# Kernel tuning notes

Hardware: AMD Instinct MI355X
Metric: run time of the kernel (lower is better)

Reference implementation:

```python
import jax, jax.numpy as jnp
from jax import lax
import numpy as np

B, N, CF = 16, 4096, 64
NPOINT, NSAMPLE = 1024, 32
MLP = (64, 64, 128)
IN_CH = CF + 3
EPS = 1e-5


def _fps(xyz, npoint):
    # Farthest point sampling; deterministic start at index 0 (original uses a random start).
    Bn = xyz.shape[0]
    d0 = jnp.full(xyz.shape[:2], 1e10, xyz.dtype)
    f0 = jnp.zeros((Bn,), jnp.int32)
    def step(carry, _):
        dist, far = carry
        c = jnp.take_along_axis(xyz, far[:, None, None], axis=1)  # (B,1,3)
        d = jnp.sum((xyz - c) ** 2, axis=-1)                      # (B,N)
        dist = jnp.minimum(dist, d)
        return (dist, jnp.argmax(dist, axis=1).astype(jnp.int32)), far
    _, idxs = lax.scan(step, (d0, f0), None, length=npoint)
    return jnp.transpose(idxs)  # (B, npoint)


def _gather(pts, idx):
    # pts (B,N,C), idx (B,...) int -> (B,...,C)
    return jax.vmap(lambda p, i: p[i])(pts, idx)


def _bn_relu(x, g, b, axes):
    # training-mode batch norm (batch statistics), channel axis = 1
    m = jnp.mean(x, axes, keepdims=True)
    v = jnp.var(x, axes, keepdims=True)
    sh = (1, -1) + (1,) * (x.ndim - 2)
    return jax.nn.relu((x - m) * lax.rsqrt(v + EPS) * g.reshape(sh) + b.reshape(sh))


def _forward(xyz, points, density, params):
    fps_idx = _fps(xyz, NPOINT)
    new_xyz = _gather(xyz, fps_idx)  # (B,S,3)
    # source query_ball_point sorts distances and keeps the nsample nearest -> kNN
    d = (jnp.sum(new_xyz ** 2, -1)[:, :, None] + jnp.sum(xyz ** 2, -1)[:, None, :]
         - 2.0 * jnp.einsum('bsc,bnc->bsn', new_xyz, xyz))  # (B,S,N)
    _, idx = lax.top_k(-d, NSAMPLE)  # (B,S,ns) nearest neighbors
    gxyz = _gather(xyz, idx) - new_xyz[:, :, None, :]           # (B,S,ns,3)
    gpts = _gather(jnp.transpose(points, (0, 2, 1)), idx)       # (B,S,ns,CF)
    x = jnp.transpose(jnp.concatenate([gxyz, gpts], -1), (0, 3, 1, 2))  # (B,IN_CH,S,ns)
    (w0, b0, g0, be0, w1, b1, g1, be1, w2, b2, g2, be2, wd, bd, gd, bed) = params
    for w, b, g, be in ((w0, b0, g0, be0), (w1, b1, g1, be1), (w2, b2, g2, be2)):
        x = _bn_relu(jnp.einsum('oc,bcsk->bosk', w, x) + b[None, :, None, None], g, be, (0, 2, 3))
    # density weighting at sampled centers
    dcen = jnp.transpose(_gather(jnp.transpose(density, (0, 2, 1)), fps_idx), (0, 2, 1))  # (B,1,S)
    dw = _bn_relu(jnp.einsum('oc,bcs->bos', wd, dcen) + bd[None, :, None], gd, bed, (0, 2))  # (B,Cout,S)
    x = x * dw[..., None]
    return new_xyz, jnp.max(x, axis=-1)  # (B,S,3), (B,Cout,S)


def setup_inputs() -> dict:
    key = jax.random.key(0)
    ks = jax.random.split(key, 3)
    inp = {
        'xyz': jax.random.normal(ks[0], (B, N, 3), jnp.float32),
        'points': jax.random.normal(ks[1], (B, CF, N), jnp.float32),
        'density': jax.random.uniform(ks[2], (B, 1, N), jnp.float32),
    }
    chans = (IN_CH,) + MLP
    for i in range(3):
        cin, cout = chans[i], chans[i + 1]
        inp[f'w{i}'] = jax.random.normal(jax.random.fold_in(key, 10 + i), (cout, cin), jnp.float32) / np.sqrt(cin).astype(np.float32)
        inp[f'b{i}'] = jnp.zeros((cout,), jnp.float32)
        inp[f'g{i}'] = jnp.ones((cout,), jnp.float32)
        inp[f'be{i}'] = jnp.zeros((cout,), jnp.float32)
    inp['wd'] = jax.random.normal(jax.random.fold_in(key, 20), (MLP[-1], 1), jnp.float32)
    inp['bd'] = jnp.zeros((MLP[-1],), jnp.float32)
    inp['gd'] = jnp.ones((MLP[-1],), jnp.float32)
    inp['bed'] = jnp.zeros((MLP[-1],), jnp.float32)
    return inp


def reference(xyz, points, density, w0, b0, g0, be0, w1, b1, g1, be1, w2, b2, g2, be2, wd, bd, gd, bed):
    return _forward(xyz, points, density,
                    (w0, b0, g0, be0, w1, b1, g1, be1, w2, b2, g2, be2, wd, bd, gd, bed))
```

## Files before the change

### kernel.cpp

```cpp
#include <hip/hip_runtime.h>
#include <hip/hip_bf16.h>
#include <stdint.h>

#define NB 16
#define NN 4096
#define NCF 64
#define NS 1024
#define NK 32
#define NPTS (NB*NS*NK)
#define CIN 67
#define EPSV 1e-5f

static __device__ __forceinline__ float fmul(float a, float b){ return __fmul_rn(a,b); }
static __device__ __forceinline__ float fadd(float a, float b){ return __fadd_rn(a,b); }
static __device__ __forceinline__ float fsub(float a, float b){ return __fsub_rn(a,b); }

typedef float f2 __attribute__((ext_vector_type(2)));
#define PK_ADD(d,a,b) asm("v_pk_add_f32 %0, %1, %2" : "=v"(d) : "v"(a), "v"(b))
#define PK_MUL(d,a,b) asm("v_pk_mul_f32 %0, %1, %2" : "=v"(d) : "v"(a), "v"(b))
static __device__ __forceinline__ f2 pk_add(f2 a, f2 b){ f2 d; PK_ADD(d,a,b); return d; }

typedef short bf16x8 __attribute__((ext_vector_type(8)));
typedef float f32x4 __attribute__((ext_vector_type(4)));

static __device__ __forceinline__ unsigned short f2b(float f){
  unsigned u = __float_as_uint(f);
  return (unsigned short)((u + 0x7FFFu + ((u>>16)&1u)) >> 16);
}
static __device__ __forceinline__ unsigned pack2(float a, float b){
  return (unsigned)f2b(a) | ((unsigned)f2b(b)<<16);
}
static __device__ __forceinline__ unsigned long long umax64(unsigned long long a,
                                                            unsigned long long b){
  return a > b ? a : b;
}

template<int CTRL>
static __device__ __forceinline__ float dppmax_f32(float x){
  float o = __uint_as_float((unsigned)__builtin_amdgcn_update_dpp(
      0, (int)__float_as_uint(x), CTRL, 0xf, 0xf, true));
  return fmaxf(x, o);
}
static __device__ __forceinline__ float wave_max63_f32(float x){
  x = dppmax_f32<0x111>(x); x = dppmax_f32<0x112>(x);
  x = dppmax_f32<0x114>(x); x = dppmax_f32<0x118>(x);
  x = dppmax_f32<0x142>(x); x = dppmax_f32<0x143>(x);
  return x;
}
template<int CTRL>
static __device__ __forceinline__ float dppmax_keep(float x){
  float o = __uint_as_float((unsigned)__builtin_amdgcn_update_dpp(
      (int)__float_as_uint(x), (int)__float_as_uint(x), CTRL, 0xf, 0xf, false));
  return fmaxf(x, o);
}
static __device__ __forceinline__ float row16_max_f32(float x){
  x = dppmax_keep<0x111>(x); x = dppmax_keep<0x112>(x);
  x = dppmax_keep<0x114>(x); x = dppmax_keep<0x118>(x);
  return x;
}
template<int CTRL>
static __device__ __forceinline__ f2 dppadd_f2(f2 x){
  f2 o;
  o.x = __uint_as_float((unsigned)__builtin_amdgcn_update_dpp(
      0, (int)__float_as_uint(x.x), CTRL, 0xf, 0xf, true));
  o.y = __uint_as_float((unsigned)__builtin_amdgcn_update_dpp(
      0, (int)__float_as_uint(x.y), CTRL, 0xf, 0xf, true));
  return pk_add(x, o);
}
static __device__ __forceinline__ f2 row16_sum_f2(f2 x){
  x = dppadd_f2<0x111>(x); x = dppadd_f2<0x112>(x);
  x = dppadd_f2<0x114>(x); x = dppadd_f2<0x118>(x);
  return x;
}
static __device__ __forceinline__ unsigned long long readlane_u64(unsigned long long v, int l){
  unsigned lo = (unsigned)__builtin_amdgcn_readlane((int)(unsigned)v, l);
  unsigned hi = (unsigned)__builtin_amdgcn_readlane((int)(unsigned)(v>>32), l);
  return ((unsigned long long)hi<<32) | lo;
}
static __device__ __forceinline__ unsigned long long wave_shr1_u64(unsigned long long x){
  unsigned lo = (unsigned)__builtin_amdgcn_update_dpp(
      0, (int)(unsigned)x, 0x138, 0xf, 0xf, true);
  unsigned hi = (unsigned)__builtin_amdgcn_update_dpp(
      0, (int)(unsigned)(x>>32), 0x138, 0xf, 0xf, true);
  return ((unsigned long long)hi<<32) | lo;
}

__global__ __launch_bounds__(256) void prep_kernel(const float* __restrict__ pts,
    const float* __restrict__ xyz, unsigned short* __restrict__ ptsT,
    float* __restrict__ sqx){
  int blk = blockIdx.x;
  int b = blk >> 4;
  int n = ((blk & 15) << 8) + threadIdx.x;
  const float* src = pts + (size_t)b*NCF*NN + n;
  float v[NCF];
  #pragma unroll
  for (int c=0;c<NCF;c++) v[c] = src[(size_t)c*NN];
  uint4* dst = (uint4*)(ptsT + ((size_t)b*NN + n)*NCF);
  #pragma unroll
  for (int j=0;j<8;j++)
    dst[j] = make_uint4(pack2(v[8*j],v[8*j+1]), pack2(v[8*j+2],v[8*j+3]),
                        pack2(v[8*j+4],v[8*j+5]), pack2(v[8*j+6],v[8*j+7]));
  const float* xp = xyz + ((size_t)b*NN + n)*3;
  float x=xp[0], y=xp[1], z=xp[2];
  sqx[(size_t)b*NN+n] = fadd(fadd(fmul(x,x),fmul(y,y)),fmul(z,z));
}

#define FT 512
__global__ __launch_bounds__(FT) void fps_kernel(const float* __restrict__ xyz,
    int* __restrict__ fidx, float* __restrict__ newxyz){
  int b = blockIdx.x;
  __shared__ float4 s4[NN];
  __shared__ unsigned long long candK[2][8];
  const int tid = threadIdx.x;
  const int lane = tid & 63;
  const int wv = tid >> 6;
  for (int i = tid; i < NN; i += FT){
    const float* p = xyz + ((size_t)b*NN + i)*3;
    s4[i] = make_float4(p[0], p[1], p[2], 0.f);
  }
  __syncthreads();
  f2 px[4], py[4], pz[4], d2[4];
  #pragma unroll
  for (int m=0;m<4;m++){
    float4 a = s4[tid*8 + 2*m];
    float4 c = s4[tid*8 + 2*m + 1];
    px[m] = (f2){a.x, c.x};
    py[m] = (f2){a.y, c.y};
    pz[m] = (f2){a.z, c.z};
    d2[m] = (f2){1e10f, 1e10f};
  }
  int far = 0;
  float4 cc = s4[0];
  for (int s=0;s<NS;s++){
    if (tid==0){
      fidx[b*NS+s] = far;
      float* o = newxyz + ((size_t)b*NS+s)*3;
      o[0]=cc.x; o[1]=cc.y; o[2]=cc.z;
    }
    f2 ncx = (f2){-cc.x,-cc.x}, ncy = (f2){-cc.y,-cc.y}, ncz = (f2){-cc.z,-cc.z};
    float bv = -1.0f; int bj = 0;
    #pragma unroll
    for (int m=0;m<4;m++){
      f2 dx,dy,dz,xx,yy,zz,ss,dd;
      PK_ADD(dx, px[m], ncx);
      PK_ADD(dy, py[m], ncy);
      PK_ADD(dz, pz[m], ncz);
      PK_MUL(xx, dx, dx);
      PK_MUL(yy, dy, dy);
      PK_ADD(ss, xx, yy);
      PK_MUL(zz, dz, dz);
      PK_ADD(dd, ss, zz);
      float u0 = fminf(d2[m].x, dd.x);
      float u1 = fminf(d2[m].y, dd.y);
      d2[m].x = u0; d2[m].y = u1;
      if (u0 > bv){ bv = u0; bj = 2*m; }
      if (u1 > bv){ bv = u1; bj = 2*m+1; }
    }
    int nbest = (tid<<3) + bj;
    float mv = wave_max63_f32(bv);
    float mvu = __uint_as_float((unsigned)__builtin_amdgcn_readlane(
        (int)__float_as_uint(mv), 63));
    unsigned long long tiedm = __ballot(bv == mvu);
    int wl = __ffsll(tiedm) - 1;
    unsigned nwin = (unsigned)__builtin_amdgcn_readlane(nbest, wl);
    if (lane == 0)
      candK[s&1][wv] = ((unsigned long long)__float_as_uint(mvu) << 32)
                     | (unsigned long long)(unsigned)~nwin;
    __syncthreads();
    const ulonglong2* cp = (const ulonglong2*)candK[s&1];
    ulonglong2 c0=cp[0], c1=cp[1], c2=cp[2], c3=cp[3];
    unsigned long long kk = umax64(
        umax64(umax64(c0.x,c0.y), umax64(c1.x,c1.y)),
        umax64(umax64(c2.x,c2.y), umax64(c3.x,c3.y)));
    far = (int)(~(unsigned)kk) & (NN-1);
    cc = s4[far];
  }
}

__global__ __launch_bounds__(256) void dcen_kernel(const float* __restrict__ density,
    const int* __restrict__ fidx, float* __restrict__ dcen){
  int i = blockIdx.x*256 + threadIdx.x;
  int b = i >> 10;
  dcen[i] = density[(size_t)b*NN + fidx[i]];
}

__global__ __launch_bounds__(256) void dstats_kernel(const float* __restrict__ dcen,
    float* __restrict__ dstat){
  float s=0.f, q=0.f;
  for (int i=threadIdx.x; i<NB*NS; i+=256){ float v=dcen[i]; s+=v; q+=v*v; }
  __shared__ float ls[256], lq[256];
  ls[threadIdx.x]=s; lq[threadIdx.x]=q;
  __syncthreads();
  for (int off=128; off>0; off>>=1){
    if (threadIdx.x<off){ ls[threadIdx.x]+=ls[threadIdx.x+off]; lq[threadIdx.x]+=lq[threadIdx.x+off]; }
    __syncthreads();
  }
  if (threadIdx.x==0){
    float m = ls[0]/(float)(NB*NS);
    dstat[0]=m; dstat[1]=lq[0]/(float)(NB*NS) - m*m;
  }
}

__global__ __launch_bounds__(256) void knn_kernel(const float* __restrict__ xyz,
    const float* __restrict__ sqx, const float* __restrict__ newxyz,
    int* __restrict__ kidx){
  const int lane = threadIdx.x & 63;
  const int g = blockIdx.x*4 + (threadIdx.x >> 6);
  const int b = g >> 10;
  const float* cp = newxyz + (size_t)g*3;
  const float cx=cp[0], cy=cp[1], cz=cp[2];
  const float sqc = fadd(fadd(fmul(cx,cx),fmul(cy,cy)),fmul(cz,cz));
  const float* xb  = xyz + (size_t)b*NN*3;
  const float* sqb = sqx + (size_t)b*NN;
  unsigned long long kept  = ~0ULL;
  unsigned long long worst = ~0ULL;
  for (int n0=0; n0<NN; n0+=64){
    const int n = n0 + lane;
    const float* xp = xb + (size_t)n*3;
    float x=xp[0], y=xp[1], z=xp[2];
    float dot = fadd(fadd(fmul(cx,x),fmul(cy,y)),fmul(cz,z));
    float d = fsub(fadd(sqc, sqb[n]), fmul(2.0f,dot));
    unsigned u = __float_as_uint(d);
    u = (u & 0x80000000u) ? ~u : (u | 0x80000000u);
    unsigned long long ck = ((unsigned long long)u << 32) | (unsigned)n;
    unsigned long long mask = __ballot(ck < worst);
    while (mask){
      const int l = __ffsll(mask) - 1;
      mask &= mask - 1;
      const unsigned long long k = readlane_u64(ck, l);
      if (k < worst){
        bool m = kept > k;
        unsigned long long M = __ballot(m) << 1;
        unsigned long long sh = wave_shr1_u64(kept);
        bool msh = (M >> lane) & 1ULL;
        unsigned long long ins = msh ? sh : k;
        kept = m ? ins : kept;
        worst = readlane_u64(kept, 31);
      }
    }
  }
  if (lane < 32) kidx[(size_t)g*NK + lane] = (int)(kept & 0xFFFFFFFFULL);
}


__global__ __launch_bounds__(256) void conv1_kernel(const float* __restrict__ xyz,
    const unsigned short* __restrict__ ptsT, const float* __restrict__ newxyz,
    const int* __restrict__ kidx, const float* __restrict__ w0,
    const float* __restrict__ b0, unsigned short* __restrict__ z1,
    float* __restrict__ partial){
  __shared__ unsigned short sa[128][104];
  __shared__ unsigned short swb[64][104];
  const int tid = threadIdx.x;
  const int p0 = blockIdx.x * 128;
  for (int i = tid; i < 64*52; i += 256){
    int o = i / 52, pr = i - o*52, c0 = 2*pr;
    float v0 = (c0 < 64) ? w0[o*CIN + 3 + c0] : (c0 < 67 ? w0[o*CIN + (c0-64)] : 0.f);
    int c1 = c0 + 1;
    float v1 = (c1 < 64) ? w0[o*CIN + 3 + c1] : (c1 < 67 ? w0[o*CIN + (c1-64)] : 0.f);
    *(unsigned*)&swb[o][c0] = pack2(v0, v1);
  }
  #pragma unroll
  for (int j=0;j<4;j++){
    int idx = tid + j*256;
    int pt = idx >> 3, cg = idx & 7;
    int p = p0 + pt, g = p >> 5, b = g >> 10;
    int n = kidx[p];
    uint4 vv = *(const uint4*)(ptsT + ((size_t)b*NN + n)*NCF + cg*8);
    *(uint4*)&sa[pt][cg*8] = vv;
  }
  if (tid < 128){
    int p = p0 + tid, g = p >> 5, b = g >> 10;
    int n = kidx[p];
    const float* xp = xyz + ((size_t)b*NN + n)*3;
    const float* cp = newxyz + (size_t)g*3;
    float gx = xp[0]-cp[0], gy = xp[1]-cp[1], gz = xp[2]-cp[2];
    *(uint2*)&sa[tid][64] = make_uint2(pack2(gx,gy), pack2(gz,0.f));
    *(uint2*)&sa[tid][68] = make_uint2(0u,0u);
    uint4 zz = make_uint4(0u,0u,0u,0u);
    *(uint4*)&sa[tid][72] = zz; *(uint4*)&sa[tid][80] = zz;
    *(uint4*)&sa[tid][88] = zz; *(uint4*)&sa[tid][96] = zz;
  }
  __syncthreads();
  const int wv = tid >> 6, lane = tid & 63;
  const int r15 = lane & 15, q = lane >> 4;
  f32x4 acc[8];
  #pragma unroll
  for (int t=0;t<8;t++) acc[t] = (f32x4){0.f,0.f,0.f,0.f};
  #pragma unroll
  for (int ks=0; ks<3; ks++){
    bf16x8 af = *(const bf16x8*)&swb[wv*16 + r15][ks*32 + q*8];
    #pragma unroll
    for (int t=0;t<8;t++){
      bf16x8 bfr = *(const bf16x8*)&sa[t*16 + r15][ks*32 + q*8];
      acc[t] = __builtin_amdgcn_mfma_f32_16x16x32_bf16(af, bfr, acc[t], 0,0,0);
    }
  }
  float bias[4];
  #pragma unroll
  for (int r=0;r<4;r++) bias[r] = b0[wv*16 + q*4 + r];
  f2 st[4];
  #pragma unroll
  for (int r=0;r<4;r++) st[r] = (f2){0.f,0.f};
  #pragma unroll
  for (int t=0;t<8;t++){
    float z0=acc[t][0]+bias[0], z1v=acc[t][1]+bias[1];
    float z2v=acc[t][2]+bias[2], z3v=acc[t][3]+bias[3];
    st[0] = pk_add(st[0], (f2){z0, z0*z0});
    st[1] = pk_add(st[1], (f2){z1v, z1v*z1v});
    st[2] = pk_add(st[2], (f2){z2v, z2v*z2v});
    st[3] = pk_add(st[3], (f2){z3v, z3v*z3v});
    *(uint2*)(z1 + (size_t)(p0 + t*16 + r15)*64 + wv*16 + q*4)
        = make_uint2(pack2(z0,z1v), pack2(z2v,z3v));
  }
  #pragma unroll
  for (int r=0;r<4;r++){
    f2 s = row16_sum_f2(st[r]);
    if (r15 == 15){
      int ch = wv*16 + q*4 + r;
      partial[(size_t)blockIdx.x*128 + ch] = s.x;
      partial[(size_t)blockIdx.x*128 + 64 + ch] = s.y;
    }
  }
}

__global__ __launch_bounds__(256) void conv2_kernel(const unsigned short* __restrict__ z1,
    const float* __restrict__ w1, const float* __restrict__ b1,
    const float* __restrict__ scale1, const float* __restrict__ shift1,
    unsigned short* __restrict__ z2, float* __restrict__ partial){
  __shared__ unsigned short sa[128][72];
  __shared__ unsigned short swb[64][72];
  const int tid = threadIdx.x;
  const int p0 = blockIdx.x * 128;
  for (int i = tid; i < 64*32; i += 256){
    int o = i >> 5, c0 = (i & 31)*2;
    *(unsigned*)&swb[o][c0] = pack2(w1[o*64+c0], w1[o*64+c0+1]);
  }
  #pragma unroll
  for (int j=0;j<4;j++){
    int idx = tid + j*256;
    int pt = idx >> 3, cg = idx & 7;
    uint4 vv = *(const uint4*)(z1 + (size_t)(p0+pt)*64 + cg*8);
    unsigned a[4] = {vv.x, vv.y, vv.z, vv.w};
    unsigned r[4];
    #pragma unroll
    for (int t=0;t<4;t++){
      int c = cg*8 + t*2;
      float lo = __uint_as_float(a[t] << 16);
      float hi = __uint_as_float(a[t] & 0xFFFF0000u);
      float alo = fmaxf(lo*scale1[c]   + shift1[c],   0.f);
      float ahi = fmaxf(hi*scale1[c+1] + shift1[c+1], 0.f);
      r[t] = pack2(alo, ahi);
    }
    *(uint4*)&sa[pt][cg*8] = make_uint4(r[0],r[1],r[2],r[3]);
  }
  __syncthreads();
  const int wv = tid >> 6, lane = tid & 63;
  const int r15 = lane & 15, q = lane >> 4;
  f32x4 acc[8];
  #pragma unroll
  for (int t=0;t<8;t++) acc[t] = (f32x4){0.f,0.f,0.f,0.f};
  #pragma unroll
  for (int ks=0; ks<2; ks++){
    bf16x8 af = *(const bf16x8*)&swb[wv*16 + r15][ks*32 + q*8];
    #pragma unroll
    for (int t=0;t<8;t++){
      bf16x8 bfr = *(const bf16x8*)&sa[t*16 + r15][ks*32 + q*8];
      acc[t] = __builtin_amdgcn_mfma_f32_16x16x32_bf16(af, bfr, acc[t], 0,0,0);
    }
  }
  float bias[4];
  #pragma unroll
  for (int r=0;r<4;r++) bias[r] = b1[wv*16 + q*4 + r];
  f2 st[4];
  #pragma unroll
  for (int r=0;r<4;r++) st[r] = (f2){0.f,0.f};
  #pragma unroll
  for (int t=0;t<8;t++){
    float z0=acc[t][0]+bias[0], z1v=acc[t][1]+bias[1];
    float z2v=acc[t][2]+bias[2], z3v=acc[t][3]+bias[3];
    st[0] = pk_add(st[0], (f2){z0, z0*z0});
    st[1] = pk_add(st[1], (f2){z1v, z1v*z1v});
    st[2] = pk_add(st[2], (f2){z2v, z2v*z2v});
    st[3] = pk_add(st[3], (f2){z3v, z3v*z3v});
    *(uint2*)(z2 + (size_t)(p0 + t*16 + r15)*64 + wv*16 + q*4)
        = make_uint2(pack2(z0,z1v), pack2(z2v,z3v));
  }
  #pragma unroll
  for (int r=0;r<4;r++){
    f2 s = row16_sum_f2(st[r]);
    if (r15 == 15){
      int ch = wv*16 + q*4 + r;
      partial[(size_t)blockIdx.x*128 + ch] = s.x;
      partial[(size_t)blockIdx.x*128 + 64 + ch] = s.y;
    }
  }
}

__global__ __launch_bounds__(256) void conv3_kernel(const unsigned short* __restrict__ z2,
    const float* __restrict__ w2, const float* __restrict__ b2,
    const float* __restrict__ scale2, const float* __restrict__ shift2,
    float* __restrict__ m3, float* __restrict__ partial){
  __shared__ unsigned short sa[128][72];
  __shared__ unsigned short swb[128][72];
  const int tid = threadIdx.x;
  const int p0 = blockIdx.x * 128;
  for (int i = tid; i < 128*32; i += 256){
    int o = i >> 5, c0 = (i & 31)*2;
    *(unsigned*)&swb[o][c0] = pack2(w2[o*64+c0], w2[o*64+c0+1]);
  }
  #pragma unroll
  for (int j=0;j<4;j++){
    int idx = tid + j*256;
    int pt = idx >> 3, cg = idx & 7;
    uint4 vv = *(const uint4*)(z2 + (size_t)(p0+pt)*64 + cg*8);
    unsigned a[4] = {vv.x, vv.y, vv.z, vv.w};
    unsigned r[4];
    #pragma unroll
    for (int t=0;t<4;t++){
      int c = cg*8 + t*2;
      float lo = __uint_as_float(a[t] << 16);
      float hi = __uint_as_float(a[t] & 0xFFFF0000u);
      float alo = fmaxf(lo*scale2[c]   + shift2[c],   0.f);
      float ahi = fmaxf(hi*scale2[c+1] + shift2[c+1], 0.f);
      r[t] = pack2(alo, ahi);
    }
    *(uint4*)&sa[pt][cg*8] = make_uint4(r[0],r[1],r[2],r[3]);
  }
  __syncthreads();
  const int wv = tid >> 6, lane = tid & 63;
  const int r15 = lane & 15, q = lane >> 4;
  f32x4 acc[2][8];
  #pragma unroll
  for (int mm=0;mm<2;mm++)
    #pragma unroll
    for (int t=0;t<8;t++) acc[mm][t] = (f32x4){0.f,0.f,0.f,0.f};
  #pragma unroll
  for (int ks=0; ks<2; ks++){
    bf16x8 af0 = *(const bf16x8*)&swb[(wv*2+0)*16 + r15][ks*32 + q*8];
    bf16x8 af1 = *(const bf16x8*)&swb[(wv*2+1)*16 + r15][ks*32 + q*8];
    #pragma unroll
    for (int t=0;t<8;t++){
      bf16x8 bfr = *(const bf16x8*)&sa[t*16 + r15][ks*32 + q*8];
      acc[0][t] = __builtin_amdgcn_mfma_f32_16x16x32_bf16(af0, bfr, acc[0][t], 0,0,0);
      acc[1][t] = __builtin_amdgcn_mfma_f32_16x16x32_bf16(af1, bfr, acc[1][t], 0,0,0);
    }
  }
  #pragma unroll
  for (int mm=0;mm<2;mm++){
    const int base = (wv*2+mm)*16;
    float bias[4];
    #pragma unroll
    for (int r=0;r<4;r++) bias[r] = b2[base + q*4 + r];
    float zv[8][4];
    f2 st[4];
    #pragma unroll
    for (int r=0;r<4;r++) st[r] = (f2){0.f,0.f};
    #pragma unroll
    for (int t=0;t<8;t++){
      #pragma unroll
      for (int r=0;r<4;r++){
        float z = acc[mm][t][r] + bias[r];
        zv[t][r] = z;
        st[r] = pk_add(st[r], (f2){z, z*z});
      }
    }
    #pragma unroll
    for (int r=0;r<4;r++){
      f2 s = row16_sum_f2(st[r]);
      if (r15 == 15){
        int ch = base + q*4 + r;
        partial[(size_t)blockIdx.x*256 + ch] = s.x;
        partial[(size_t)blockIdx.x*256 + 128 + ch] = s.y;
      }
    }
    #pragma unroll
    for (int c=0;c<4;c++){
      #pragma unroll
      for (int r=0;r<4;r++){
        float m = row16_max_f32(fmaxf(zv[2*c][r], zv[2*c+1][r]));
        if (r15 == 15)
          m3[(size_t)(blockIdx.x*4 + c)*128 + base + q*4 + r] = m;
      }
    }
  }
}

__global__ __launch_bounds__(256) void mkbn_kernel(const float* __restrict__ partial,
    int nrows, int stride, const float* __restrict__ g, const float* __restrict__ be,
    float* __restrict__ scale, float* __restrict__ shift, float inv_count){
  const int c = blockIdx.x;
  const int C = gridDim.x;
  float s=0.f, q=0.f;
  for (int r=threadIdx.x; r<nrows; r+=256){
    s += partial[(size_t)r*stride + c];
    q += partial[(size_t)r*stride + C + c];
  }
  __shared__ float ls[256], lq[256];
  ls[threadIdx.x]=s; lq[threadIdx.x]=q;
  __syncthreads();
  for (int off=128; off>0; off>>=1){
    if (threadIdx.x < off){ ls[threadIdx.x]+=ls[threadIdx.x+off]; lq[threadIdx.x]+=lq[threadIdx.x+off]; }
    __syncthreads();
  }
  if (threadIdx.x==0){
    float mean = ls[0]*inv_count;
    float var  = lq[0]*inv_count - mean*mean;
    float sc = g[c]*rsqrtf(var + EPSV);
    scale[c]=sc; shift[c]=be[c]-mean*sc;
  }
}

__global__ __launch_bounds__(256) void final_kernel(const float* __restrict__ m3,
    const float* __restrict__ dcen, const float* __restrict__ scale3,
    const float* __restrict__ shift3, const float* __restrict__ wd,
    const float* __restrict__ bd, const float* __restrict__ gd,
    const float* __restrict__ bed, const float* __restrict__ dstat,
    float* __restrict__ out){
  size_t i = (size_t)blockIdx.x*256 + threadIdx.x;
  int s  = (int)(i & 1023);
  int ch = (int)((i >> 10) & 127);
  int b  = (int)(i >> 17);
  float mean_d = dstat[0], var_d = dstat[1];
  float w = wd[ch];
  float meanp = w*mean_d + bd[ch];
  float varp  = w*w*var_d;
  float dsc = gd[ch]*rsqrtf(varp + EPSV);
  float dsh = bed[ch] - meanp*dsc;
  float pre = w*dcen[b*NS+s] + bd[ch];
  float dw  = fmaxf(dsc*pre + dsh, 0.0f);
  float z   = m3[((size_t)(b*NS+s))*128 + ch];
  float x   = fmaxf(scale3[ch]*z + shift3[ch], 0.0f);
  out[i] = x*dw;
}

extern "C" void kernel_launch(void* const* d_in, const int* in_sizes, int n_in,
                              void* d_out, int out_size, void* d_ws, size_t ws_size,
                              hipStream_t stream){
  const float* xyz     = (const float*)d_in[0];
  const float* points  = (const float*)d_in[1];
  const float* density = (const float*)d_in[2];
  const float* w0 = (const float*)d_in[3];
  const float* b0 = (const float*)d_in[4];
  const float* g0 = (const float*)d_in[5];
  const float* be0= (const float*)d_in[6];
  const float* w1 = (const float*)d_in[7];
  const float* b1 = (const float*)d_in[8];
  const float* g1 = (const float*)d_in[9];
  const float* be1= (const float*)d_in[10];
  const float* w2 = (const float*)d_in[11];
  const float* b2 = (const float*)d_in[12];
  const float* g2 = (const float*)d_in[13];
  const float* be2= (const float*)d_in[14];
  const float* wd = (const float*)d_in[15];
  const float* bd = (const float*)d_in[16];
  const float* gd = (const float*)d_in[17];
  const float* bed= (const float*)d_in[18];

  float* out = (float*)d_out;
  float* newxyz = out;
  float* out1   = out + (size_t)NB*NS*3;

  unsigned short* ptsT = (unsigned short*)d_ws;
  float* sqx  = (float*)(ptsT + (size_t)NB*NN*NCF);
  int*   fidx = (int*)(sqx + (size_t)NB*NN);
  float* dcen = (float*)(fidx + NB*NS);
  int*   kidx = (int*)(dcen + NB*NS);
  unsigned short* z1 = (unsigned short*)(kidx + NPTS);
  unsigned short* z2 = z1 + (size_t)NPTS*64;
  float* m3   = (float*)(z2 + (size_t)NPTS*64);
  float* p1   = m3 + (size_t)NB*NS*128;
  float* p2   = p1 + 4096*128;
  float* p3   = p2 + 4096*128;
  float* bnp  = p3 + 4096*256;
  float* dstat= bnp + 512;

  hipLaunchKernelGGL(prep_kernel,  dim3(256),  dim3(256), 0, stream, points, xyz, ptsT, sqx);
  hipLaunchKernelGGL(fps_kernel,   dim3(NB),   dim3(FT),  0, stream, xyz, fidx, newxyz);
  hipLaunchKernelGGL(dcen_kernel,  dim3(64),   dim3(256), 0, stream, density, fidx, dcen);
  hipLaunchKernelGGL(dstats_kernel,dim3(1),    dim3(256), 0, stream, dcen, dstat);
  hipLaunchKernelGGL(knn_kernel,   dim3(4096), dim3(256), 0, stream, xyz, sqx, newxyz, kidx);
  hipLaunchKernelGGL(conv1_kernel, dim3(4096), dim3(256), 0, stream, xyz, ptsT, newxyz, kidx, w0, b0, z1, p1);
  hipLaunchKernelGGL(mkbn_kernel,  dim3(64),   dim3(256), 0, stream, p1, 4096, 128, g0, be0, bnp+0,   bnp+64,  1.0f/(float)NPTS);
  hipLaunchKernelGGL(conv2_kernel, dim3(4096), dim3(256), 0, stream, z1, w1, b1, bnp+0, bnp+64, z2, p2);
  hipLaunchKernelGGL(mkbn_kernel,  dim3(64),   dim3(256), 0, stream, p2, 4096, 128, g1, be1, bnp+128, bnp+192, 1.0f/(float)NPTS);
  hipLaunchKernelGGL(conv3_kernel, dim3(4096), dim3(256), 0, stream, z2, w2, b2, bnp+128, bnp+192, m3, p3);
  hipLaunchKernelGGL(mkbn_kernel,  dim3(128),  dim3(256), 0, stream, p3, 4096, 256, g2, be2, bnp+256, bnp+384, 1.0f/(float)NPTS);
  hipLaunchKernelGGL(final_kernel, dim3(8192), dim3(256), 0, stream, m3, dcen, bnp+256, bnp+384, wd, bd, gd, bed, dstat, out1);
}
```

Measured before the change: 1.137 ms.

## Shrink FPS block, carry winner coords via readlane, prepack bf16 weights, transpose m3

The FPS kernel drops to 256 threads with 16 points each. The winning point's coordinates are now passed through the shared candidate records, which removes the dependent shared-memory load of s4[far] on the serial critical path. Conv weights are converted to bf16 once in a new wprep kernel, so each of the 4096 conv blocks no longer repacks them. The m3 buffer is stored channel-major so the final kernel reads it coalesced, at the cost of scattered writes in conv3.

```diff
diff --git a/kernel.cpp b/kernel.cpp
--- a/kernel.cpp
+++ b/kernel.cpp
@@ -30,9 +30,8 @@
 static __device__ __forceinline__ unsigned pack2(float a, float b){
   return (unsigned)f2b(a) | ((unsigned)f2b(b)<<16);
 }
-static __device__ __forceinline__ unsigned long long umax64(unsigned long long a,
-                                                            unsigned long long b){
-  return a > b ? a : b;
+static __device__ __forceinline__ float readlane_f32(float v, int l){
+  return __uint_as_float((unsigned)__builtin_amdgcn_readlane((int)__float_as_uint(v), l));
 }
 
 template<int CTRL>
@@ -105,12 +104,29 @@
   sqx[(size_t)b*NN+n] = fadd(fadd(fmul(x,x),fmul(y,y)),fmul(z,z));
 }
 
-#define FT 512
+__global__ __launch_bounds__(256) void wprep_kernel(const float* __restrict__ w0,
+    const float* __restrict__ w1, const float* __restrict__ w2,
+    unsigned short* __restrict__ w0p, unsigned short* __restrict__ w1p,
+    unsigned short* __restrict__ w2p){
+  const int tid = threadIdx.x;
+  for (int i = tid; i < 64*128; i += 256){
+    int o = i >> 7, c = i & 127;
+    float v = 0.f;
+    if (c < 64) v = w0[o*CIN + 3 + c];
+    else if (c < 67) v = w0[o*CIN + (c-64)];
+    w0p[i] = f2b(v);
+  }
+  for (int i = tid; i < 64*64; i += 256)  w1p[i] = f2b(w1[i]);
+  for (int i = tid; i < 128*64; i += 256) w2p[i] = f2b(w2[i]);
+}
+
+#define FT 256
 __global__ __launch_bounds__(FT) void fps_kernel(const float* __restrict__ xyz,
     int* __restrict__ fidx, float* __restrict__ newxyz){
   int b = blockIdx.x;
   __shared__ float4 s4[NN];
-  __shared__ unsigned long long candK[2][8];
+  __shared__ ulonglong2 candA[2][4];
+  __shared__ float4 candZ[2];
   const int tid = threadIdx.x;
   const int lane = tid & 63;
   const int wv = tid >> 6;
@@ -119,28 +135,28 @@
     s4[i] = make_float4(p[0], p[1], p[2], 0.f);
   }
   __syncthreads();
-  f2 px[4], py[4], pz[4], d2[4];
-  #pragma unroll
-  for (int m=0;m<4;m++){
-    float4 a = s4[tid*8 + 2*m];
-    float4 c = s4[tid*8 + 2*m + 1];
+  f2 px[8], py[8], pz[8], d2[8];
+  #pragma unroll
+  for (int m=0;m<8;m++){
+    float4 a = s4[tid*16 + 2*m];
+    float4 c = s4[tid*16 + 2*m + 1];
     px[m] = (f2){a.x, c.x};
     py[m] = (f2){a.y, c.y};
     pz[m] = (f2){a.z, c.z};
     d2[m] = (f2){1e10f, 1e10f};
   }
   int far = 0;
-  float4 cc = s4[0];
+  float ccx = s4[0].x, ccy = s4[0].y, ccz = s4[0].z;
   for (int s=0;s<NS;s++){
     if (tid==0){
       fidx[b*NS+s] = far;
       float* o = newxyz + ((size_t)b*NS+s)*3;
-      o[0]=cc.x; o[1]=cc.y; o[2]=cc.z;
-    }
-    f2 ncx = (f2){-cc.x,-cc.x}, ncy = (f2){-cc.y,-cc.y}, ncz = (f2){-cc.z,-cc.z};
+      o[0]=ccx; o[1]=ccy; o[2]=ccz;
+    }
+    f2 ncx = (f2){-ccx,-ccx}, ncy = (f2){-ccy,-ccy}, ncz = (f2){-ccz,-ccz};
     float bv = -1.0f; int bj = 0;
     #pragma unroll
-    for (int m=0;m<4;m++){
+    for (int m=0;m<8;m++){
       f2 dx,dy,dz,xx,yy,zz,ss,dd;
       PK_ADD(dx, px[m], ncx);
       PK_ADD(dy, py[m], ncy);
@@ -156,24 +172,56 @@
       if (u0 > bv){ bv = u0; bj = 2*m; }
       if (u1 > bv){ bv = u1; bj = 2*m+1; }
     }
-    int nbest = (tid<<3) + bj;
+    int nbest = (tid<<4) + bj;
     float mv = wave_max63_f32(bv);
-    float mvu = __uint_as_float((unsigned)__builtin_amdgcn_readlane(
-        (int)__float_as_uint(mv), 63));
+    float mvu = readlane_f32(mv, 63);
     unsigned long long tiedm = __ballot(bv == mvu);
     int wl = __ffsll(tiedm) - 1;
     unsigned nwin = (unsigned)__builtin_amdgcn_readlane(nbest, wl);
-    if (lane == 0)
-      candK[s&1][wv] = ((unsigned long long)__float_as_uint(mvu) << 32)
-                     | (unsigned long long)(unsigned)~nwin;
+    int bjw = (int)(nwin & 15);
+    int mW = bjw >> 1;
+    f2 pxw, pyw, pzw;
+    switch(mW){
+      case 0: pxw=px[0]; pyw=py[0]; pzw=pz[0]; break;
+      case 1: pxw=px[1]; pyw=py[1]; pzw=pz[1]; break;
+      case 2: pxw=px[2]; pyw=py[2]; pzw=pz[2]; break;
+      case 3: pxw=px[3]; pyw=py[3]; pzw=pz[3]; break;
+      case 4: pxw=px[4]; pyw=py[4]; pzw=pz[4]; break;
+      case 5: pxw=px[5]; pyw=py[5]; pzw=pz[5]; break;
+      case 6: pxw=px[6]; pyw=py[6]; pzw=pz[6]; break;
+      default: pxw=px[7]; pyw=py[7]; pzw=pz[7]; break;
+    }
+    bool hi = (bjw & 1) != 0;
+    float cxw = readlane_f32(hi ? pxw.y : pxw.x, wl);
+    float cyw = readlane_f32(hi ? pyw.y : pyw.x, wl);
+    float czw = readlane_f32(hi ? pzw.y : pzw.x, wl);
+    if (lane == 0){
+      unsigned long long key = ((unsigned long long)__float_as_uint(mvu) << 32)
+                             | (unsigned long long)(unsigned)~nwin;
+      unsigned long long cxy = ((unsigned long long)__float_as_uint(cyw) << 32)
+                             | (unsigned long long)__float_as_uint(cxw);
+      candA[s&1][wv] = (ulonglong2){key, cxy};
+      ((float*)&candZ[s&1])[wv] = czw;
+    }
     __syncthreads();
-    const ulonglong2* cp = (const ulonglong2*)candK[s&1];
-    ulonglong2 c0=cp[0], c1=cp[1], c2=cp[2], c3=cp[3];
-    unsigned long long kk = umax64(
-        umax64(umax64(c0.x,c0.y), umax64(c1.x,c1.y)),
-        umax64(umax64(c2.x,c2.y), umax64(c3.x,c3.y)));
+    ulonglong2 A0 = candA[s&1][0], A1 = candA[s&1][1];
+    ulonglong2 A2 = candA[s&1][2], A3 = candA[s&1][3];
+    float4 Z = candZ[s&1];
+    bool a01 = A1.x > A0.x;
+    unsigned long long k01 = a01 ? A1.x : A0.x;
+    unsigned long long xy01 = a01 ? A1.y : A0.y;
+    float z01 = a01 ? Z.y : Z.x;
+    bool a23 = A3.x > A2.x;
+    unsigned long long k23 = a23 ? A3.x : A2.x;
+    unsigned long long xy23 = a23 ? A3.y : A2.y;
+    float z23 = a23 ? Z.w : Z.z;
+    bool af = k23 > k01;
+    unsigned long long kk = af ? k23 : k01;
+    unsigned long long xyf = af ? xy23 : xy01;
+    ccz = af ? z23 : z01;
+    ccx = __uint_as_float((unsigned)xyf);
+    ccy = __uint_as_float((unsigned)(xyf >> 32));
     far = (int)(~(unsigned)kk) & (NN-1);
-    cc = s4[far];
   }
 }
 
@@ -245,19 +293,17 @@
 
 __global__ __launch_bounds__(256) void conv1_kernel(const float* __restrict__ xyz,
     const unsigned short* __restrict__ ptsT, const float* __restrict__ newxyz,
-    const int* __restrict__ kidx, const float* __restrict__ w0,
+    const int* __restrict__ kidx, const unsigned short* __restrict__ w0p,
     const float* __restrict__ b0, unsigned short* __restrict__ z1,
     float* __restrict__ partial){
   __shared__ unsigned short sa[128][104];
   __shared__ unsigned short swb[64][104];
   const int tid = threadIdx.x;
   const int p0 = blockIdx.x * 128;
-  for (int i = tid; i < 64*52; i += 256){
-    int o = i / 52, pr = i - o*52, c0 = 2*pr;
-    float v0 = (c0 < 64) ? w0[o*CIN + 3 + c0] : (c0 < 67 ? w0[o*CIN + (c0-64)] : 0.f);
-    int c1 = c0 + 1;
-    float v1 = (c1 < 64) ? w0[o*CIN + 3 + c1] : (c1 < 67 ? w0[o*CIN + (c1-64)] : 0.f);
-    *(unsigned*)&swb[o][c0] = pack2(v0, v1);
+  for (int i = tid; i < 64*64; i += 256){
+    int o = i >> 6, c0 = (i & 63)*2;
+    if (c0 < 104)
+      *(unsigned*)&swb[o][c0] = *(const unsigned*)&w0p[o*128 + c0];
   }
   #pragma unroll
   for (int j=0;j<4;j++){
@@ -324,7 +370,7 @@
 }
 
 __global__ __launch_bounds__(256) void conv2_kernel(const unsigned short* __restrict__ z1,
-    const float* __restrict__ w1, const float* __restrict__ b1,
+    const unsigned short* __restrict__ w1p, const float* __restrict__ b1,
     const float* __restrict__ scale1, const float* __restrict__ shift1,
     unsigned short* __restrict__ z2, float* __restrict__ partial){
   __shared__ unsigned short sa[128][72];
@@ -333,7 +379,7 @@
   const int p0 = blockIdx.x * 128;
   for (int i = tid; i < 64*32; i += 256){
     int o = i >> 5, c0 = (i & 31)*2;
-    *(unsigned*)&swb[o][c0] = pack2(w1[o*64+c0], w1[o*64+c0+1]);
+    *(unsigned*)&swb[o][c0] = *(const unsigned*)&w1p[o*64 + c0];
   }
   #pragma unroll
   for (int j=0;j<4;j++){
@@ -397,16 +443,16 @@
 }
 
 __global__ __launch_bounds__(256) void conv3_kernel(const unsigned short* __restrict__ z2,
-    const float* __restrict__ w2, const float* __restrict__ b2,
+    const unsigned short* __restrict__ w2p, const float* __restrict__ b2,
     const float* __restrict__ scale2, const float* __restrict__ shift2,
-    float* __restrict__ m3, float* __restrict__ partial){
+    float* __restrict__ m3T, float* __restrict__ partial){
   __shared__ unsigned short sa[128][72];
   __shared__ unsigned short swb[128][72];
   const int tid = threadIdx.x;
   const int p0 = blockIdx.x * 128;
   for (int i = tid; i < 128*32; i += 256){
     int o = i >> 5, c0 = (i & 31)*2;
-    *(unsigned*)&swb[o][c0] = pack2(w2[o*64+c0], w2[o*64+c0+1]);
+    *(unsigned*)&swb[o][c0] = *(const unsigned*)&w2p[o*64 + c0];
   }
   #pragma unroll
   for (int j=0;j<4;j++){
@@ -479,7 +525,7 @@
       for (int r=0;r<4;r++){
         float m = row16_max_f32(fmaxf(zv[2*c][r], zv[2*c+1][r]));
         if (r15 == 15)
-          m3[(size_t)(blockIdx.x*4 + c)*128 + base + q*4 + r] = m;
+          m3T[(size_t)(base + q*4 + r)*(NB*NS) + blockIdx.x*4 + c] = m;
       }
     }
   }
@@ -510,7 +556,7 @@
   }
 }
 
-__global__ __launch_bounds__(256) void final_kernel(const float* __restrict__ m3,
+__global__ __launch_bounds__(256) void final_kernel(const float* __restrict__ m3T,
     const float* __restrict__ dcen, const float* __restrict__ scale3,
     const float* __restrict__ shift3, const float* __restrict__ wd,
     const float* __restrict__ bd, const float* __restrict__ gd,
@@ -528,7 +574,7 @@
   float dsh = bed[ch] - meanp*dsc;
   float pre = w*dcen[b*NS+s] + bd[ch];
   float dw  = fmaxf(dsc*pre + dsh, 0.0f);
-  float z   = m3[((size_t)(b*NS+s))*128 + ch];
+  float z   = m3T[(size_t)ch*(NB*NS) + b*NS + s];
   float x   = fmaxf(scale3[ch]*z + shift3[ch], 0.0f);
   out[i] = x*dw;
 }
@@ -567,23 +613,27 @@
   int*   kidx = (int*)(dcen + NB*NS);
   unsigned short* z1 = (unsigned short*)(kidx + NPTS);
   unsigned short* z2 = z1 + (size_t)NPTS*64;
-  float* m3   = (float*)(z2 + (size_t)NPTS*64);
-  float* p1   = m3 + (size_t)NB*NS*128;
+  float* m3T  = (float*)(z2 + (size_t)NPTS*64);
+  float* p1   = m3T + (size_t)NB*NS*128;
   float* p2   = p1 + 4096*128;
   float* p3   = p2 + 4096*128;
   float* bnp  = p3 + 4096*256;
   float* dstat= bnp + 512;
+  unsigned short* w0p = (unsigned short*)(dstat + 2);
+  unsigned short* w1p = w0p + 64*128;
+  unsigned short* w2p = w1p + 64*64;
 
   hipLaunchKernelGGL(prep_kernel,  dim3(256),  dim3(256), 0, stream, points, xyz, ptsT, sqx);
+  hipLaunchKernelGGL(wprep_kernel, dim3(1),    dim3(256), 0, stream, w0, w1, w2, w0p, w1p, w2p);
   hipLaunchKernelGGL(fps_kernel,   dim3(NB),   dim3(FT),  0, stream, xyz, fidx, newxyz);
   hipLaunchKernelGGL(dcen_kernel,  dim3(64),   dim3(256), 0, stream, density, fidx, dcen);
   hipLaunchKernelGGL(dstats_kernel,dim3(1),    dim3(256), 0, stream, dcen, dstat);
   hipLaunchKernelGGL(knn_kernel,   dim3(4096), dim3(256), 0, stream, xyz, sqx, newxyz, kidx);
-  hipLaunchKernelGGL(conv1_kernel, dim3(4096), dim3(256), 0, stream, xyz, ptsT, newxyz, kidx, w0, b0, z1, p1);
+  hipLaunchKernelGGL(conv1_kernel, dim3(4096), dim3(256), 0, stream, xyz, ptsT, newxyz, kidx, w0p, b0, z1, p1);
   hipLaunchKernelGGL(mkbn_kernel,  dim3(64),   dim3(256), 0, stream, p1, 4096, 128, g0, be0, bnp+0,   bnp+64,  1.0f/(float)NPTS);
-  hipLaunchKernelGGL(conv2_kernel, dim3(4096), dim3(256), 0, stream, z1, w1, b1, bnp+0, bnp+64, z2, p2);
+  hipLaunchKernelGGL(conv2_kernel, dim3(4096), dim3(256), 0, stream, z1, w1p, b1, bnp+0, bnp+64, z2, p2);
   hipLaunchKernelGGL(mkbn_kernel,  dim3(64),   dim3(256), 0, stream, p2, 4096, 128, g1, be1, bnp+128, bnp+192, 1.0f/(float)NPTS);
-  hipLaunchKernelGGL(conv3_kernel, dim3(4096), dim3(256), 0, stream, z2, w2, b2, bnp+128, bnp+192, m3, p3);
+  hipLaunchKernelGGL(conv3_kernel, dim3(4096), dim3(256), 0, stream, z2, w2p, b2, bnp+128, bnp+192, m3T, p3);
   hipLaunchKernelGGL(mkbn_kernel,  dim3(128),  dim3(256), 0, stream, p3, 4096, 256, g2, be2, bnp+256, bnp+384, 1.0f/(float)NPTS);
-  hipLaunchKernelGGL(final_kernel, dim3(8192), dim3(256), 0, stream, m3, dcen, bnp+256, bnp+384, wd, bd, gd, bed, dstat, out1);
-}
+  hipLaunchKernelGGL(final_kernel, dim3(8192), dim3(256), 0, stream, m3T, dcen, bnp+256, bnp+384, wd, bd, gd, bed, dstat, out1);
+}
```

New measurement: 1.298 ms. +14.2%, slower.
